# Kernel optimization log

Hardware: AMD Instinct MI355X
Metric: run time of the kernel (lower is better)

## Reference

```python
import jax, jax.numpy as jnp
import numpy as np

SEQ, BATCH, IN_DIM, HID, NQ = 256, 512, 512, 512, 32


def setup_inputs() -> dict:
    key = jax.random.key(0)
    k_in, k_fw, k_fb, k_ow, k_ob = jax.random.split(key, 5)
    s_fc = 1.0 / np.sqrt(IN_DIM + HID)
    s_out = 1.0 / np.sqrt(NQ)
    return {
        "inputs": jax.random.normal(k_in, (SEQ, BATCH, IN_DIM), dtype=jnp.float32),
        "fc_w": jax.random.uniform(k_fw, (NQ, IN_DIM + HID), jnp.float32, -s_fc, s_fc),
        "fc_b": jax.random.uniform(k_fb, (NQ,), jnp.float32, -s_fc, s_fc),
        "out_w": jax.random.uniform(k_ow, (HID, NQ), jnp.float32, -s_out, s_out),
        "out_b": jax.random.uniform(k_ob, (HID,), jnp.float32, -s_out, s_out),
    }


def _quantum_gate(q_in):
    # RX(x_i) on wire i then CNOT ladder; <Z_k> = prod_{j<=k} cos(x_j)
    return jnp.cumprod(jnp.cos(q_in), axis=-1)


def reference(inputs, fc_w, fc_b, out_w, out_b):
    batch = inputs.shape[1]
    h0 = jnp.zeros((batch, HID), dtype=inputs.dtype)
    c0 = jnp.zeros((batch, HID), dtype=inputs.dtype)

    def step(carry, x):
        hx, cx = carry
        combined = jnp.concatenate([x, hx], axis=1)            # [B, IN+HID]
        q_in = combined @ fc_w.T + fc_b                        # [B, NQ]
        q = _quantum_gate(q_in)                                # [B, NQ]
        f = jax.nn.sigmoid(q) @ out_w.T + out_b                # [B, HID]
        i = f                                                  # same circuit & weights as f
        g = jnp.tanh(q) @ out_w.T + out_b
        o = f                                                  # same as f
        cx = f * cx + i * g
        hx = o * jnp.tanh(cx)
        return (hx, cx), hx

    (hx, cx), outputs = jax.lax.scan(step, (h0, c0), inputs)
    return outputs, hx, cx
```

## Files before the change

### kernel.cpp

```cpp
#include <hip/hip_runtime.h>
#include <math.h>

#define SEQ 256
#define BATCH 512
#define IN_DIM 512
#define HID 512
#define NQ 32

typedef float v2f __attribute__((ext_vector_type(2)));

__device__ __forceinline__ float fast_rcp(float x) { return __builtin_amdgcn_rcpf(x); }

__device__ __forceinline__ float tanh_fast(float x) {
    float a = fabsf(x);
    float e = __expf(-2.0f * a);
    float r = (1.0f - e) * fast_rcp(1.0f + e);
    return copysignf(r, x);
}

template <int CTRL>
__device__ __forceinline__ float dpp_add(float x) {
    int t = __builtin_amdgcn_update_dpp(0, __float_as_int(x), CTRL, 0xF, 0xF, false);
    return x + __int_as_float(t);
}
__device__ __forceinline__ float reduce16_add(float x) {
    x = dpp_add<0xB1>(x);
    x = dpp_add<0x4E>(x);
    x = dpp_add<0x141>(x);
    x = dpp_add<0x140>(x);
    return x;
}
template <int CTRL, int ROW_MASK>
__device__ __forceinline__ float dpp_mul1(float x) {
    int t = __builtin_amdgcn_update_dpp(0x3f800000 , __float_as_int(x),
                                        CTRL, ROW_MASK, 0xF, false);
    return x * __int_as_float(t);
}
__device__ __forceinline__ float scan32_mul(float x) {
    x = dpp_mul1<0x111, 0xF>(x);
    x = dpp_mul1<0x112, 0xF>(x);
    x = dpp_mul1<0x114, 0xF>(x);
    x = dpp_mul1<0x118, 0xF>(x);
    x = dpp_mul1<0x142, 0xA>(x);
    return x;
}

__global__ __launch_bounds__(256, 4) void xp_kernel(const float* __restrict__ x,
                                                    const float* __restrict__ fc_w,
                                                    const float* __restrict__ fc_b,
                                                    float* __restrict__ xp) {
    const int tid = threadIdx.x;
    const int g2 = tid >> 4;
    const int s  = tid & 15;

    __shared__ float4 tile4[16 * 128];

    v2f wA_lo[8], wA_hi[8], wB_lo[8], wB_hi[8];
    {
        const float* wrA = fc_w + (size_t)(g2 * 2 + 0) * (IN_DIM + HID) + 4 * s;
        const float* wrB = fc_w + (size_t)(g2 * 2 + 1) * (IN_DIM + HID) + 4 * s;
#pragma unroll
        for (int j = 0; j < 8; ++j) {
            float4 a = *reinterpret_cast<const float4*>(wrA + 64 * j);
            float4 b = *reinterpret_cast<const float4*>(wrB + 64 * j);
            wA_lo[j] = (v2f){a.x, a.y}; wA_hi[j] = (v2f){a.z, a.w};
            wB_lo[j] = (v2f){b.x, b.y}; wB_hi[j] = (v2f){b.z, b.w};
        }
    }
    const float2 bias2 = reinterpret_cast<const float2*>(fc_b)[g2];

    const float4* x4 = reinterpret_cast<const float4*>(x) + (size_t)blockIdx.x * (16 * 128);
#pragma unroll
    for (int q = 0; q < 8; ++q)
        tile4[tid + 256 * q] = x4[tid + 256 * q];
    __syncthreads();

    const int row0 = blockIdx.x * 16;
    float2* xp2 = reinterpret_cast<float2*>(xp);
    for (int rp = 0; rp < 8; ++rp) {
        const int r0 = 2 * rp, r1 = 2 * rp + 1;
        v2f aA0 = (v2f){0.f, 0.f}, aA1 = aA0, aB0 = aA0, aB1 = aA0;
        v2f bA0 = aA0, bA1 = aA0, bB0 = aA0, bB1 = aA0;
#pragma unroll
        for (int j = 0; j < 8; j += 2) {
            float4 h0 = tile4[r0 * 128 + s + 16 * j];
            float4 h1 = tile4[r1 * 128 + s + 16 * j];
            v2f h0lo = (v2f){h0.x, h0.y}, h0hi = (v2f){h0.z, h0.w};
            v2f h1lo = (v2f){h1.x, h1.y}, h1hi = (v2f){h1.z, h1.w};
            aA0 = __builtin_elementwise_fma(h0lo, wA_lo[j], aA0);
            aA0 = __builtin_elementwise_fma(h0hi, wA_hi[j], aA0);
            aA1 = __builtin_elementwise_fma(h0lo, wB_lo[j], aA1);
            aA1 = __builtin_elementwise_fma(h0hi, wB_hi[j], aA1);
            aB0 = __builtin_elementwise_fma(h1lo, wA_lo[j], aB0);
            aB0 = __builtin_elementwise_fma(h1hi, wA_hi[j], aB0);
            aB1 = __builtin_elementwise_fma(h1lo, wB_lo[j], aB1);
            aB1 = __builtin_elementwise_fma(h1hi, wB_hi[j], aB1);
            float4 g0 = tile4[r0 * 128 + s + 16 * (j + 1)];
            float4 g1 = tile4[r1 * 128 + s + 16 * (j + 1)];
            v2f g0lo = (v2f){g0.x, g0.y}, g0hi = (v2f){g0.z, g0.w};
            v2f g1lo = (v2f){g1.x, g1.y}, g1hi = (v2f){g1.z, g1.w};
            bA0 = __builtin_elementwise_fma(g0lo, wA_lo[j + 1], bA0);
            bA0 = __builtin_elementwise_fma(g0hi, wA_hi[j + 1], bA0);
            bA1 = __builtin_elementwise_fma(g0lo, wB_lo[j + 1], bA1);
            bA1 = __builtin_elementwise_fma(g0hi, wB_hi[j + 1], bA1);
            bB0 = __builtin_elementwise_fma(g1lo, wA_lo[j + 1], bB0);
            bB0 = __builtin_elementwise_fma(g1hi, wA_hi[j + 1], bB0);
            bB1 = __builtin_elementwise_fma(g1lo, wB_lo[j + 1], bB1);
            bB1 = __builtin_elementwise_fma(g1hi, wB_hi[j + 1], bB1);
        }
        v2f sA0 = aA0 + bA0, sA1 = aA1 + bA1, sB0 = aB0 + bB0, sB1 = aB1 + bB1;
        float rA0 = reduce16_add(sA0.x + sA0.y);
        float rA1 = reduce16_add(sA1.x + sA1.y);
        float rB0 = reduce16_add(sB0.x + sB0.y);
        float rB1 = reduce16_add(sB1.x + sB1.y);
        if (s == 0) {
            xp2[(size_t)(row0 + r0) * 16 + g2] = make_float2(rA0 + bias2.x, rA1 + bias2.y);
            xp2[(size_t)(row0 + r1) * 16 + g2] = make_float2(rB0 + bias2.x, rB1 + bias2.y);
        }
    }
}

__global__ __launch_bounds__(256, 2) void rnn_kernel(const float* __restrict__ xp,
                                                     const float* __restrict__ fc_w,
                                                     const float* __restrict__ out_w,
                                                     const float* __restrict__ out_b,
                                                     float* __restrict__ out) {
    const int b = blockIdx.x;
    const int tid = threadIdx.x;
    const int g = tid >> 4;
    const int s = tid & 15;
    const int w4 = tid >> 6;
    const int lane = tid & 63;
    const int l31 = lane & 31;

    __shared__ __align__(16) float hbuf[2][HID];
    __shared__ __align__(16) float qin_s[NQ];
    __shared__ __align__(16) float wbuf[4][64];
    __shared__ __align__(16) float xps[SEQ * NQ];

    v2f whA_lo[8], whA_hi[8], whB_lo[8], whB_hi[8];
    {
        const float* wrA = fc_w + (size_t)(g * 2 + 0) * (IN_DIM + HID) + IN_DIM + 4 * s;
        const float* wrB = fc_w + (size_t)(g * 2 + 1) * (IN_DIM + HID) + IN_DIM + 4 * s;
#pragma unroll
        for (int j = 0; j < 8; ++j) {
            float4 a = *reinterpret_cast<const float4*>(wrA + 64 * j);
            float4 c = *reinterpret_cast<const float4*>(wrB + 64 * j);
            whA_lo[j] = (v2f){a.x, a.y}; whA_hi[j] = (v2f){a.z, a.w};
            whB_lo[j] = (v2f){c.x, c.y}; whB_hi[j] = (v2f){c.z, c.w};
        }
    }
    float ow0[NQ], ow1[NQ];
    {
        const float4* o0 = reinterpret_cast<const float4*>(out_w + (size_t)tid * NQ);
        const float4* o1 = reinterpret_cast<const float4*>(out_w + (size_t)(tid + 256) * NQ);
#pragma unroll
        for (int q4 = 0; q4 < 8; ++q4) {
            float4 a = o0[q4], bq = o1[q4];
            ow0[4 * q4 + 0] = a.x;  ow0[4 * q4 + 1] = a.y;
            ow0[4 * q4 + 2] = a.z;  ow0[4 * q4 + 3] = a.w;
            ow1[4 * q4 + 0] = bq.x; ow1[4 * q4 + 1] = bq.y;
            ow1[4 * q4 + 2] = bq.z; ow1[4 * q4 + 3] = bq.w;
        }
    }
    const float ob0 = out_b[tid];
    const float ob1 = out_b[tid + 256];

    {
        const float4* xpg = reinterpret_cast<const float4*>(xp);
        float4* xps4 = reinterpret_cast<float4*>(xps);
#pragma unroll
        for (int k = 0; k < 8; ++k) {
            int idx = tid + 256 * k;
            int t = idx >> 3, q4 = idx & 7;
            xps4[idx] = xpg[((size_t)t * BATCH + b) * 8 + q4];
        }
    }
    hbuf[0][tid] = 0.0f;
    hbuf[0][tid + 256] = 0.0f;
    float c0 = 0.0f, c1 = 0.0f;
    __syncthreads();

    float* hx_out = out + (size_t)SEQ * BATCH * HID + (size_t)b * HID;
    float* cx_out = hx_out + (size_t)BATCH * HID;

    int p = 0;
    for (int t = 0; t < SEQ; ++t) {
        const float2 xq = reinterpret_cast<const float2*>(xps)[t * 16 + g];
        const float4* h4 = reinterpret_cast<const float4*>(hbuf[p]);
        v2f aA = (v2f){0.f, 0.f}, aB = aA, bA = aA, bB = aA;
#pragma unroll
        for (int j = 0; j < 8; j += 2) {
            float4 hv = h4[s + 16 * j];
            v2f hlo = (v2f){hv.x, hv.y}, hhi = (v2f){hv.z, hv.w};
            aA = __builtin_elementwise_fma(hlo, whA_lo[j], aA);
            aA = __builtin_elementwise_fma(hhi, whA_hi[j], aA);
            aB = __builtin_elementwise_fma(hlo, whB_lo[j], aB);
            aB = __builtin_elementwise_fma(hhi, whB_hi[j], aB);
            float4 gv = h4[s + 16 * (j + 1)];
            v2f glo = (v2f){gv.x, gv.y}, ghi = (v2f){gv.z, gv.w};
            bA = __builtin_elementwise_fma(glo, whA_lo[j + 1], bA);
            bA = __builtin_elementwise_fma(ghi, whA_hi[j + 1], bA);
            bB = __builtin_elementwise_fma(glo, whB_lo[j + 1], bB);
            bB = __builtin_elementwise_fma(ghi, whB_hi[j + 1], bB);
        }
        v2f sA = aA + bA, sB = aB + bB;
        float rA = reduce16_add(sA.x + sA.y);
        float rB = reduce16_add(sB.x + sB.y);
        if (s == 0)
            reinterpret_cast<float2*>(qin_s)[g] = make_float2(rA + xq.x, rB + xq.y);
        __syncthreads();

        {
            float q = qin_s[l31];
            float pp = scan32_mul(__cosf(q));
            float arg = (lane < 32) ? -pp : (-2.0f * pp);
            float e = __expf(arg);
            float num = (lane < 32) ? 1.0f : (1.0f - e);
            float val = num * fast_rcp(1.0f + e);
            wbuf[w4][(l31 << 1) | (lane >> 5)] = val;
        }
        asm volatile("s_waitcnt lgkmcnt(0)" ::: "memory");
        __builtin_amdgcn_sched_barrier(0);

        const float4* st4 = reinterpret_cast<const float4*>(wbuf[w4]);
        v2f a0 = (v2f){ob0, ob0};
        v2f a1 = (v2f){ob1, ob1};
#pragma unroll
        for (int m = 0; m < 16; ++m) {
            float4 v = st4[m];
            v2f plo = (v2f){v.x, v.y}, phi = (v2f){v.z, v.w};
            a0 = __builtin_elementwise_fma(plo, (v2f){ow0[2 * m], ow0[2 * m]}, a0);
            a0 = __builtin_elementwise_fma(phi, (v2f){ow0[2 * m + 1], ow0[2 * m + 1]}, a0);
            a1 = __builtin_elementwise_fma(plo, (v2f){ow1[2 * m], ow1[2 * m]}, a1);
            a1 = __builtin_elementwise_fma(phi, (v2f){ow1[2 * m + 1], ow1[2 * m + 1]}, a1);
        }
        float f0 = a0.x, g0 = a0.y, f1 = a1.x, g1 = a1.y;
        c0 = f0 * (c0 + g0);
        c1 = f1 * (c1 + g1);
        float h0 = f0 * tanh_fast(c0);
        float h1 = f1 * tanh_fast(c1);

        hbuf[p ^ 1][tid] = h0;
        hbuf[p ^ 1][tid + 256] = h1;
        float* orow = out + ((size_t)t * BATCH + b) * HID;
        orow[tid] = h0;
        orow[tid + 256] = h1;
        if (t == SEQ - 1) {
            hx_out[tid] = h0; hx_out[tid + 256] = h1;
            cx_out[tid] = c0; cx_out[tid + 256] = c1;
        }
        __syncthreads();
        p ^= 1;
    }
}

extern "C" void kernel_launch(void* const* d_in, const int* in_sizes, int n_in,
                              void* d_out, int out_size, void* d_ws, size_t ws_size,
                              hipStream_t stream) {
    const float* inputs = (const float*)d_in[0];
    const float* fc_w   = (const float*)d_in[1];
    const float* fc_b   = (const float*)d_in[2];
    const float* out_w  = (const float*)d_in[3];
    const float* out_b  = (const float*)d_in[4];
    float* out = (float*)d_out;
    float* xp  = (float*)d_ws;

    xp_kernel<<<(SEQ * BATCH) / 16, 256, 0, stream>>>(inputs, fc_w, fc_b, xp);
    rnn_kernel<<<BATCH, 256, 0, stream>>>(xp, fc_w, out_w, out_b, out);
}
```

Before: 378.8 us.

## Partition recurrent matvec by wave-owned hidden slices to drop one block barrier per step

```diff
diff --git a/kernel.cpp b/kernel.cpp
--- a/kernel.cpp
+++ b/kernel.cpp
@@ -28,6 +28,11 @@
     x = dpp_add<0x4E>(x);
     x = dpp_add<0x141>(x);
     x = dpp_add<0x140>(x);
+    return x;
+}
+__device__ __forceinline__ float reduce4_add(float x) {
+    x = dpp_add<0xB1>(x);
+    x = dpp_add<0x4E>(x);
     return x;
 }
 template <int CTRL, int ROW_MASK>
@@ -44,6 +49,13 @@
     x = dpp_mul1<0x142, 0xA>(x);
     return x;
 }
+
+#define BLOCK_BARRIER_LDS() asm volatile("s_waitcnt lgkmcnt(0)\n\ts_barrier" ::: "memory")
+#define WAVE_FENCE_LDS()                                        \
+    do {                                                        \
+        asm volatile("s_waitcnt lgkmcnt(0)" ::: "memory");      \
+        __builtin_amdgcn_sched_barrier(0);                      \
+    } while (0)
 
 __global__ __launch_bounds__(256, 4) void xp_kernel(const float* __restrict__ x,
                                                     const float* __restrict__ fc_w,
@@ -127,33 +139,36 @@
                                                      float* __restrict__ out) {
     const int b = blockIdx.x;
     const int tid = threadIdx.x;
-    const int g = tid >> 4;
-    const int s = tid & 15;
     const int w4 = tid >> 6;
     const int lane = tid & 63;
     const int l31 = lane & 31;
-
-    __shared__ __align__(16) float hbuf[2][HID];
-    __shared__ __align__(16) float qin_s[NQ];
+    const int grp = lane >> 2;
+    const int sl = lane & 3;
+
+    __shared__ __align__(16) float hbuf[HID];
+    __shared__ __align__(16) float pbuf[2][4][NQ];
     __shared__ __align__(16) float wbuf[4][64];
     __shared__ __align__(16) float xps[SEQ * NQ];
 
     v2f whA_lo[8], whA_hi[8], whB_lo[8], whB_hi[8];
     {
-        const float* wrA = fc_w + (size_t)(g * 2 + 0) * (IN_DIM + HID) + IN_DIM + 4 * s;
-        const float* wrB = fc_w + (size_t)(g * 2 + 1) * (IN_DIM + HID) + IN_DIM + 4 * s;
+        const int kbase = IN_DIM + 128 * w4 + 32 * sl;
+        const float* wrA = fc_w + (size_t)(grp * 2 + 0) * (IN_DIM + HID) + kbase;
+        const float* wrB = fc_w + (size_t)(grp * 2 + 1) * (IN_DIM + HID) + kbase;
 #pragma unroll
         for (int j = 0; j < 8; ++j) {
-            float4 a = *reinterpret_cast<const float4*>(wrA + 64 * j);
-            float4 c = *reinterpret_cast<const float4*>(wrB + 64 * j);
+            float4 a = *reinterpret_cast<const float4*>(wrA + 4 * j);
+            float4 c = *reinterpret_cast<const float4*>(wrB + 4 * j);
             whA_lo[j] = (v2f){a.x, a.y}; whA_hi[j] = (v2f){a.z, a.w};
             whB_lo[j] = (v2f){c.x, c.y}; whB_hi[j] = (v2f){c.z, c.w};
         }
     }
+    const int hid0 = 128 * w4 + lane;
+    const int hid1 = hid0 + 64;
     float ow0[NQ], ow1[NQ];
     {
-        const float4* o0 = reinterpret_cast<const float4*>(out_w + (size_t)tid * NQ);
-        const float4* o1 = reinterpret_cast<const float4*>(out_w + (size_t)(tid + 256) * NQ);
+        const float4* o0 = reinterpret_cast<const float4*>(out_w + (size_t)hid0 * NQ);
+        const float4* o1 = reinterpret_cast<const float4*>(out_w + (size_t)hid1 * NQ);
 #pragma unroll
         for (int q4 = 0; q4 < 8; ++q4) {
             float4 a = o0[q4], bq = o1[q4];
@@ -163,8 +178,8 @@
             ow1[4 * q4 + 2] = bq.z; ow1[4 * q4 + 3] = bq.w;
         }
     }
-    const float ob0 = out_b[tid];
-    const float ob1 = out_b[tid + 256];
+    const float ob0 = out_b[hid0];
+    const float ob1 = out_b[hid1];
 
     {
         const float4* xpg = reinterpret_cast<const float4*>(xp);
@@ -176,28 +191,28 @@
             xps4[idx] = xpg[((size_t)t * BATCH + b) * 8 + q4];
         }
     }
-    hbuf[0][tid] = 0.0f;
-    hbuf[0][tid + 256] = 0.0f;
+    hbuf[tid] = 0.0f;
+    hbuf[tid + 256] = 0.0f;
     float c0 = 0.0f, c1 = 0.0f;
     __syncthreads();
 
     float* hx_out = out + (size_t)SEQ * BATCH * HID + (size_t)b * HID;
     float* cx_out = hx_out + (size_t)BATCH * HID;
 
-    int p = 0;
+    const float4* h4 = reinterpret_cast<const float4*>(hbuf) + (32 * w4 + 8 * sl);
+
+    int par = 0;
     for (int t = 0; t < SEQ; ++t) {
-        const float2 xq = reinterpret_cast<const float2*>(xps)[t * 16 + g];
-        const float4* h4 = reinterpret_cast<const float4*>(hbuf[p]);
         v2f aA = (v2f){0.f, 0.f}, aB = aA, bA = aA, bB = aA;
 #pragma unroll
         for (int j = 0; j < 8; j += 2) {
-            float4 hv = h4[s + 16 * j];
+            float4 hv = h4[j];
             v2f hlo = (v2f){hv.x, hv.y}, hhi = (v2f){hv.z, hv.w};
             aA = __builtin_elementwise_fma(hlo, whA_lo[j], aA);
             aA = __builtin_elementwise_fma(hhi, whA_hi[j], aA);
             aB = __builtin_elementwise_fma(hlo, whB_lo[j], aB);
             aB = __builtin_elementwise_fma(hhi, whB_hi[j], aB);
-            float4 gv = h4[s + 16 * (j + 1)];
+            float4 gv = h4[j + 1];
             v2f glo = (v2f){gv.x, gv.y}, ghi = (v2f){gv.z, gv.w};
             bA = __builtin_elementwise_fma(glo, whA_lo[j + 1], bA);
             bA = __builtin_elementwise_fma(ghi, whA_hi[j + 1], bA);
@@ -205,23 +220,25 @@
             bB = __builtin_elementwise_fma(ghi, whB_hi[j + 1], bB);
         }
         v2f sA = aA + bA, sB = aB + bB;
-        float rA = reduce16_add(sA.x + sA.y);
-        float rB = reduce16_add(sB.x + sB.y);
-        if (s == 0)
-            reinterpret_cast<float2*>(qin_s)[g] = make_float2(rA + xq.x, rB + xq.y);
-        __syncthreads();
+        float rA = reduce4_add(sA.x + sA.y);
+        float rB = reduce4_add(sB.x + sB.y);
+        if (sl == 0)
+            *reinterpret_cast<float2*>(&pbuf[par][w4][2 * grp]) = make_float2(rA, rB);
+
+        BLOCK_BARRIER_LDS();
 
         {
-            float q = qin_s[l31];
-            float pp = scan32_mul(__cosf(q));
+            const float* pb = &pbuf[par][0][0];
+            float qin = (pb[l31] + pb[32 + l31]) + (pb[64 + l31] + pb[96 + l31])
+                      + xps[t * NQ + l31];
+            float pp = scan32_mul(__cosf(qin));
             float arg = (lane < 32) ? -pp : (-2.0f * pp);
             float e = __expf(arg);
             float num = (lane < 32) ? 1.0f : (1.0f - e);
             float val = num * fast_rcp(1.0f + e);
             wbuf[w4][(l31 << 1) | (lane >> 5)] = val;
         }
-        asm volatile("s_waitcnt lgkmcnt(0)" ::: "memory");
-        __builtin_amdgcn_sched_barrier(0);
+        WAVE_FENCE_LDS();
 
         const float4* st4 = reinterpret_cast<const float4*>(wbuf[w4]);
         v2f a0 = (v2f){ob0, ob0};
@@ -241,17 +258,17 @@
         float h0 = f0 * tanh_fast(c0);
         float h1 = f1 * tanh_fast(c1);
 
-        hbuf[p ^ 1][tid] = h0;
-        hbuf[p ^ 1][tid + 256] = h1;
+        hbuf[hid0] = h0;
+        hbuf[hid1] = h1;
         float* orow = out + ((size_t)t * BATCH + b) * HID;
-        orow[tid] = h0;
-        orow[tid + 256] = h1;
+        orow[hid0] = h0;
+        orow[hid1] = h1;
         if (t == SEQ - 1) {
-            hx_out[tid] = h0; hx_out[tid + 256] = h1;
-            cx_out[tid] = c0; cx_out[tid + 256] = c1;
-        }
-        __syncthreads();
-        p ^= 1;
+            hx_out[hid0] = h0; hx_out[hid1] = h1;
+            cx_out[hid0] = c0; cx_out[hid1] = c1;
+        }
+        WAVE_FENCE_LDS();
+        par ^= 1;
     }
 }
 
```

Result: faster. 369.7 us (-2.4%).
